# Kernel tuning notes

Measured on AMD Instinct MI355X. Metric: run time of the kernel, lower is better.

The kernel has to match this reference:

```python
import jax, jax.numpy as jnp
import numpy as np

N_NODES = 50000


def _gcn_layer(x, edge_index, W, b, relu):
    """tf_geometric-style GCN: h = D^-1/2 (A+I) D^-1/2 (x @ W) + b, opt relu."""
    n = x.shape[0]
    h = x @ W  # [N, D_out] transform first (standard GCN)
    src, dst = edge_index[0], edge_index[1]
    sl = jnp.arange(n, dtype=src.dtype)
    src = jnp.concatenate([src, sl])  # add self-loops (renorm trick)
    dst = jnp.concatenate([dst, sl])
    deg = jax.ops.segment_sum(jnp.ones_like(dst, dtype=h.dtype), dst, num_segments=n)
    dinv = jax.lax.rsqrt(jnp.maximum(deg, 1e-12))
    norm = dinv[src] * dinv[dst]  # symmetric normalization per edge
    msg = h[src] * norm[:, None]  # [E+N, D_out] gather + scale
    out = jax.ops.segment_sum(msg, dst, num_segments=n) + b
    return jax.nn.relu(out) if relu else out


def setup_inputs() -> dict:
    key = jax.random.key(0)
    ks = jax.random.split(key, 12)
    F, E = 512, 800000
    d = {}
    d["x"] = jax.random.normal(ks[0], (N_NODES, F), dtype=jnp.float32)
    d["edge_index1"] = jax.random.randint(ks[1], (2, E), 0, N_NODES, dtype=jnp.int32)
    d["edge_index2"] = jax.random.randint(ks[2], (2, E), 0, N_NODES, dtype=jnp.int32)
    def glorot(k, shape):
        lim = np.sqrt(6.0 / (shape[0] + shape[1])).astype(np.float32)
        return jax.random.uniform(k, shape, jnp.float32, -lim, lim)
    d["W10"] = glorot(ks[3], (F, 256)); d["b10"] = jnp.zeros((256,), jnp.float32)
    d["W20"] = glorot(ks[4], (F, 64));  d["b20"] = jnp.zeros((64,), jnp.float32)
    d["W21"] = glorot(ks[5], (64, 256)); d["b21"] = jnp.zeros((256,), jnp.float32)
    d["Wfc"] = glorot(ks[6], (256, 16)); d["bfc"] = jnp.zeros((16,), jnp.float32)
    return d


def reference(x, edge_index1, edge_index2, W10, b10, W20, b20, W21, b21, Wfc, bfc):
    h1 = _gcn_layer(x, edge_index1, W10, b10, relu=True)   # GCN(256, relu)
    h2 = _gcn_layer(x, edge_index2, W20, b20, relu=False)  # GCN(64)
    h2 = _gcn_layer(h2, edge_index2, W21, b21, relu=True)  # GCN(256, relu)
    h = h1 + h2
    return h @ Wfc + bfc  # Dense(class_num)
```

## Files before the change

kernel.cpp:

```cpp
#include <hip/hip_runtime.h>
#include <hip/hip_bf16.h>
#include <cstdint>
#include <cstddef>

#define N_NODES 50000
#define FDIM 512
#define NBKT 391
#define CHUNK 8192
#define BCAP 4096

typedef __bf16 bf16_t;
typedef bf16_t bf16x8 __attribute__((ext_vector_type(8)));
typedef float f32x4 __attribute__((ext_vector_type(4)));

__device__ __forceinline__ unsigned short f2bf(float f) {
  union { float f; uint32_t u; } c; c.f = f;
  uint32_t u = c.u;
  uint32_t r = (u + 0x7fffu + ((u >> 16) & 1u)) >> 16;
  return (unsigned short)r;
}
__device__ __forceinline__ float bf2f(unsigned short u) {
  union { uint32_t i; float f; } c; c.i = (uint32_t)u << 16; return c.f;
}
__device__ __forceinline__ float4 ld_bf4(const unsigned short* p) {
  ushort4 u = *(const ushort4*)p;
  float4 r; r.x = bf2f(u.x); r.y = bf2f(u.y); r.z = bf2f(u.z); r.w = bf2f(u.w);
  return r;
}
__device__ __forceinline__ void async16(const void* g, void* l) {
  __builtin_amdgcn_global_load_lds((const __attribute__((address_space(1))) void*)g,
                                   (__attribute__((address_space(3))) void*)l, 16, 0, 0);
}

__global__ __launch_bounds__(256) void binA(const int* __restrict__ d1, const int* __restrict__ d2,
                                            int* __restrict__ M1, int* __restrict__ M2,
                                            int E1, int E2, int nch1, int nch2) {
  const int g = blockIdx.y;
  const int* dst = g ? d2 : d1;
  int* M = g ? M2 : M1;
  const int E = g ? E2 : E1;
  const int nch = g ? nch2 : nch1;
  const int chunk = blockIdx.x;
  if (chunk >= nch) return;
  __shared__ int cnt[NBKT];
  for (int j = threadIdx.x; j < NBKT; j += 256) cnt[j] = 0;
  __syncthreads();
  const int base = chunk * CHUNK;
#pragma unroll 4
  for (int i = 0; i < CHUNK / 256; i++) {
    int e = base + i * 256 + threadIdx.x;
    if (e < E) atomicAdd(&cnt[dst[e] >> 7], 1);
  }
  __syncthreads();
  for (int j = threadIdx.x; j < NBKT; j += 256) M[chunk * NBKT + j] = cnt[j];
}

__global__ __launch_bounds__(512) void bin_offsets(int* __restrict__ M1, int* __restrict__ M2,
                                                   int* __restrict__ bases,
                                                   int nch1, int nch2, int E1, int E2) {
  const int g = blockIdx.x;
  int* M = g ? M2 : M1;
  const int nch = g ? nch2 : nch1;
  int* base = bases + g * (NBKT + 1);
  const int E = g ? E2 : E1;
  const int t = threadIdx.x;
  __shared__ int tot[512];
  int running = 0;
  if (t < NBKT) {
#pragma unroll 4
    for (int b = 0; b < nch; b++) {
      int v = M[b * NBKT + t];
      M[b * NBKT + t] = running;
      running += v;
    }
  }
  tot[t] = (t < NBKT) ? running : 0;
  __syncthreads();
  for (int off = 1; off < 512; off <<= 1) {
    int u = (t >= off) ? tot[t - off] : 0;
    __syncthreads();
    tot[t] += u;
    __syncthreads();
  }
  int ex = (t == 0) ? 0 : tot[t - 1];
  if (t < NBKT) {
    base[t] = ex;
#pragma unroll 4
    for (int b = 0; b < nch; b++) M[b * NBKT + t] += ex;
  }
  if (t == NBKT) base[NBKT] = E;
}

__global__ __launch_bounds__(256) void binB(const int* __restrict__ s1, const int* __restrict__ d1,
                                            const int* __restrict__ M1, unsigned* __restrict__ eb1,
                                            int E1, int nch1,
                                            const int* __restrict__ s2, const int* __restrict__ d2,
                                            const int* __restrict__ M2, unsigned* __restrict__ eb2,
                                            int E2, int nch2) {
  const int g = blockIdx.y;
  const int* src = g ? s2 : s1;
  const int* dst = g ? d2 : d1;
  const int* M = g ? M2 : M1;
  unsigned* eb = g ? eb2 : eb1;
  const int E = g ? E2 : E1;
  const int nch = g ? nch2 : nch1;
  const int chunk = blockIdx.x;
  if (chunk >= nch) return;
  __shared__ int gbase[NBKT];
  __shared__ int cur[NBKT];
  for (int j = threadIdx.x; j < NBKT; j += 256) {
    gbase[j] = M[chunk * NBKT + j];
    cur[j] = 0;
  }
  __syncthreads();
  const int base = chunk * CHUNK;
#pragma unroll 4
  for (int i = 0; i < CHUNK / 256; i++) {
    int e = base + i * 256 + threadIdx.x;
    if (e < E) {
      int d = dst[e];
      int b = d >> 7;
      int pos = gbase[b] + atomicAdd(&cur[b], 1);
      eb[pos] = ((unsigned)d << 16) | (unsigned)src[e];
    }
  }
}

__global__ __launch_bounds__(256) void binC(const unsigned* __restrict__ eb1,
                                            const unsigned* __restrict__ eb2,
                                            const int* __restrict__ bases,
                                            int* __restrict__ rp1, float* __restrict__ dv1,
                                            int* __restrict__ cs1,
                                            int* __restrict__ rp2, float* __restrict__ dv2,
                                            int* __restrict__ cs2, int n) {
  const int g = blockIdx.y;
  const unsigned* eb = g ? eb2 : eb1;
  const int* base = bases + g * (NBKT + 1);
  int* rp = g ? rp2 : rp1;
  float* dv = g ? dv2 : dv1;
  int* cs = g ? cs2 : cs1;
  const int bkt = blockIdx.x;
  const int e0 = base[bkt], e1 = base[bkt + 1];
  const int cnt = e1 - e0;
  const int node0 = bkt << 7;
  const int t = threadIdx.x;
  __shared__ unsigned stage[BCAP];
  __shared__ int sorted[BCAP];
  __shared__ int dcnt[128], dcur[128], dscan[128];
  if (t < 128) dcnt[t] = 0;
  __syncthreads();
  for (int i = t; i < cnt; i += 256) {
    unsigned pe = eb[e0 + i];
    stage[i] = pe;
    atomicAdd(&dcnt[(pe >> 16) & 127], 1);
  }
  __syncthreads();
  if (t < 128) dscan[t] = dcnt[t];
  __syncthreads();
  for (int off = 1; off < 128; off <<= 1) {
    int u = (t < 128 && t >= off) ? dscan[t - off] : 0;
    __syncthreads();
    if (t < 128) dscan[t] += u;
    __syncthreads();
  }
  if (t < 128) {
    int ex = dscan[t] - dcnt[t];
    dcur[t] = ex;
    int node = node0 + t;
    if (node < n) {
      rp[node] = e0 + ex;
      dv[node] = rsqrtf((float)dcnt[t] + 1.0f);
    }
  }
  __syncthreads();
  for (int i = t; i < cnt; i += 256) {
    unsigned pe = stage[i];
    int d = (pe >> 16) & 127;
    int pos = atomicAdd(&dcur[d], 1);
    sorted[pos] = (int)(pe & 0xFFFFu);
  }
  __syncthreads();
  for (int i = t; i < cnt; i += 256) cs[e0 + i] = sorted[i];
  if (bkt == NBKT - 1 && t == 0) rp[n] = base[NBKT];
}

__global__ void cvt_w(const float* __restrict__ W10, const float* __restrict__ W20,
                      const float* __restrict__ W21, unsigned short* __restrict__ WcatT,
                      unsigned short* __restrict__ W21T) {
  int j = blockIdx.x * 256 + threadIdx.x;
  const int T1 = 384 * 512;
  if (j < T1) {
    int n = j >> 9, k = j & 511;
    float v = (n < 256) ? W10[k * 256 + n] : ((n < 320) ? W20[k * 64 + (n - 256)] : 0.f);
    WcatT[j] = f2bf(v);
  } else {
    int j2 = j - T1;
    if (j2 < 256 * 64) {
      int n = j2 >> 6, k = j2 & 63;
      W21T[j2] = f2bf(W21[k * 256 + n]);
    }
  }
}

__global__ __launch_bounds__(256) void g2(const float* __restrict__ X,
                                          const unsigned short* __restrict__ B,
                                          unsigned short* __restrict__ o1,
                                          unsigned short* __restrict__ o2, int M) {
  __shared__ __attribute__((aligned(16))) unsigned short As[64 * 64];
  __shared__ __attribute__((aligned(16))) unsigned short Bs[320 * 64];
  const int tid = threadIdx.x;
  const int w = tid >> 6, lane = tid & 63;
  const int row0 = blockIdx.x * 64;
  const int mlane = lane & 15, q = lane >> 4;

  const int ar = tid >> 4;
  const int ac4 = tid & 15;

  f32x4 acc[4][5];
#pragma unroll
  for (int mi = 0; mi < 4; mi++)
#pragma unroll
    for (int ni = 0; ni < 5; ni++) {
      f32x4 z = {0.f, 0.f, 0.f, 0.f};
      acc[mi][ni] = z;
    }

  for (int k0 = 0; k0 < 512; k0 += 64) {
    __syncthreads();
    float4 areg[4];
#pragma unroll
    for (int i = 0; i < 4; i++) {
      int r = i * 16 + ar;
      int gr = row0 + r; if (gr > M - 1) gr = M - 1;
      areg[i] = *(const float4*)(X + (size_t)gr * 512 + k0 + ac4 * 4);
    }
#pragma unroll
    for (int i = 0; i < 10; i++) {
      int idx = i * 256 + tid;
      int rw = idx >> 3, c8 = idx & 7;
      int sslot = c8 ^ (rw & 7);
      async16(B + (size_t)rw * 512 + k0 + sslot * 8, &Bs[idx * 8]);
    }
#pragma unroll
    for (int i = 0; i < 4; i++) {
      int r = i * 16 + ar;
      ushort4 o;
      o.x = f2bf(areg[i].x); o.y = f2bf(areg[i].y);
      o.z = f2bf(areg[i].z); o.w = f2bf(areg[i].w);
      int slot = ((ac4 >> 1) ^ (r & 7));
      *(ushort4*)&As[r * 64 + slot * 8 + (ac4 & 1) * 4] = o;
    }
    __syncthreads();
#pragma unroll
    for (int kk = 0; kk < 2; kk++) {
      bf16x8 af[4], bfr[5];
#pragma unroll
      for (int mi = 0; mi < 4; mi++) {
        int r = mi * 16 + mlane;
        int slot = (kk * 4 + q) ^ (r & 7);
        af[mi] = *(const bf16x8*)&As[r * 64 + slot * 8];
      }
#pragma unroll
      for (int ni = 0; ni < 5; ni++) {
        int r = w * 80 + ni * 16 + mlane;
        int slot = (kk * 4 + q) ^ (r & 7);
        bfr[ni] = *(const bf16x8*)&Bs[r * 64 + slot * 8];
      }
#pragma unroll
      for (int mi = 0; mi < 4; mi++)
#pragma unroll
        for (int ni = 0; ni < 5; ni++)
          acc[mi][ni] = __builtin_amdgcn_mfma_f32_16x16x32_bf16(af[mi], bfr[ni], acc[mi][ni], 0, 0, 0);
    }
  }

#pragma unroll
  for (int mi = 0; mi < 4; mi++)
#pragma unroll
    for (int ni = 0; ni < 5; ni++) {
      int c = w * 80 + ni * 16 + mlane;
#pragma unroll
      for (int rg = 0; rg < 4; rg++) {
        int r = row0 + mi * 16 + q * 4 + rg;
        if (r < M) {
          float v = acc[mi][ni][rg];
          if (c < 256) o1[(size_t)r * 256 + c] = f2bf(v);
          else o2[(size_t)r * 64 + (c - 256)] = f2bf(v);
        }
      }
    }
}

__global__ __launch_bounds__(256) void prop256(const unsigned short* __restrict__ H,
                                               const int* __restrict__ rp,
                                               const int* __restrict__ cs,
                                               const float* __restrict__ dinv,
                                               const float* __restrict__ bias,
                                               float* __restrict__ out, int n) {
  const int i = blockIdx.x * 4 + (threadIdx.x >> 6);
  const int l = threadIdx.x & 63;
  if (i >= n) return;
  const float di = dinv[i];
  float4 self = ld_bf4(H + (size_t)i * 256 + l * 4);
  float4 acc;
  acc.x = di * self.x; acc.y = di * self.y; acc.z = di * self.z; acc.w = di * self.w;
  const int e1 = rp[i + 1];
#pragma unroll 4
  for (int e = rp[i]; e < e1; e++) {
    int s = cs[e];
    float wgt = dinv[s];
    float4 rrow = ld_bf4(H + (size_t)s * 256 + l * 4);
    acc.x += wgt * rrow.x; acc.y += wgt * rrow.y; acc.z += wgt * rrow.z; acc.w += wgt * rrow.w;
  }
  float4 b = *(const float4*)(bias + l * 4);
  float4 o;
  o.x = fmaxf(di * acc.x + b.x, 0.f);
  o.y = fmaxf(di * acc.y + b.y, 0.f);
  o.z = fmaxf(di * acc.z + b.z, 0.f);
  o.w = fmaxf(di * acc.w + b.w, 0.f);
  *(float4*)(out + (size_t)i * 256 + l * 4) = o;
}

template <int BIAS>
__global__ __launch_bounds__(256) void prop64(const unsigned short* __restrict__ H,
                                              const int* __restrict__ rp,
                                              const int* __restrict__ cs,
                                              const float* __restrict__ dinv,
                                              const float* __restrict__ bias,
                                              unsigned short* __restrict__ out, int n) {
  const int i = blockIdx.x * 16 + (threadIdx.x >> 4);
  const int l = threadIdx.x & 15;
  if (i >= n) return;
  const float di = dinv[i];
  float4 self = ld_bf4(H + (size_t)i * 64 + l * 4);
  float4 acc;
  acc.x = di * self.x; acc.y = di * self.y; acc.z = di * self.z; acc.w = di * self.w;
  const int e1 = rp[i + 1];
#pragma unroll 4
  for (int e = rp[i]; e < e1; e++) {
    int s = cs[e];
    float wgt = dinv[s];
    float4 rrow = ld_bf4(H + (size_t)s * 64 + l * 4);
    acc.x += wgt * rrow.x; acc.y += wgt * rrow.y; acc.z += wgt * rrow.z; acc.w += wgt * rrow.w;
  }
  float4 o;
  o.x = di * acc.x; o.y = di * acc.y; o.z = di * acc.z; o.w = di * acc.w;
  if (BIAS) {
    float4 b = *(const float4*)(bias + l * 4);
    o.x += b.x; o.y += b.y; o.z += b.z; o.w += b.w;
  }
  ushort4 ob;
  ob.x = f2bf(o.x); ob.y = f2bf(o.y); ob.z = f2bf(o.z); ob.w = f2bf(o.w);
  *(ushort4*)(out + (size_t)i * 64 + l * 4) = ob;
}

__global__ __launch_bounds__(512) void gf(const unsigned short* __restrict__ A,
                                          const unsigned short* __restrict__ Bb,
                                          const float* __restrict__ h1,
                                          const float* __restrict__ b21,
                                          const float* __restrict__ Wfc,
                                          const float* __restrict__ bfc,
                                          float* __restrict__ out, int M) {
  __shared__ __attribute__((aligned(16))) float hsm[128 * 260];
  __shared__ __attribute__((aligned(16))) float wt[256 * 16];
  unsigned short* As = (unsigned short*)hsm;
  unsigned short* Bs = As + 128 * 64;
  const int tid = threadIdx.x;
  const int w = tid >> 6, lane = tid & 63;
  const int row0 = blockIdx.x * 128;
  const int wm = w >> 2, wn = w & 3;
  const int mlane = lane & 15, q = lane >> 4;

  for (int j = tid; j < 4096; j += 512) wt[j] = Wfc[j];
#pragma unroll
  for (int i = 0; i < 2; i++) {
    int gr = row0 + i * 64 + w * 8 + (lane >> 3);
    if (gr > M - 1) gr = M - 1;
    async16(A + (size_t)gr * 64 + (lane & 7) * 8, &As[(i * 64 + w * 8) * 64]);
  }
#pragma unroll
  for (int i = 0; i < 4; i++) {
    int n = i * 64 + w * 8 + (lane >> 3);
    async16(Bb + (size_t)n * 64 + (lane & 7) * 8, &Bs[(i * 64 + w * 8) * 64]);
  }
  __syncthreads();

  f32x4 acc[4][4];
#pragma unroll
  for (int mi = 0; mi < 4; mi++)
#pragma unroll
    for (int ni = 0; ni < 4; ni++) {
      f32x4 z = {0.f, 0.f, 0.f, 0.f};
      acc[mi][ni] = z;
    }
#pragma unroll
  for (int kk = 0; kk < 2; kk++) {
    bf16x8 af[4], bfr[4];
#pragma unroll
    for (int mi = 0; mi < 4; mi++)
      af[mi] = *(const bf16x8*)&As[(wm * 64 + mi * 16 + mlane) * 64 + kk * 32 + q * 8];
#pragma unroll
    for (int ni = 0; ni < 4; ni++)
      bfr[ni] = *(const bf16x8*)&Bs[(wn * 64 + ni * 16 + mlane) * 64 + kk * 32 + q * 8];
#pragma unroll
    for (int mi = 0; mi < 4; mi++)
#pragma unroll
      for (int ni = 0; ni < 4; ni++)
        acc[mi][ni] = __builtin_amdgcn_mfma_f32_16x16x32_bf16(af[mi], bfr[ni], acc[mi][ni], 0, 0, 0);
  }
  __syncthreads();

#pragma unroll
  for (int ni = 0; ni < 4; ni++) {
    int c = wn * 64 + ni * 16 + mlane;
    float bb = b21[c];
#pragma unroll
    for (int mi = 0; mi < 4; mi++)
#pragma unroll
      for (int rg = 0; rg < 4; rg++) {
        int rl = wm * 64 + mi * 16 + q * 4 + rg;
        int gr = row0 + rl;
        int grc = (gr < M) ? gr : (M - 1);
        float v = fmaxf(acc[mi][ni][rg] + bb, 0.f) + h1[(size_t)grc * 256 + c];
        hsm[rl * 260 + c] = v;
      }
  }
  __syncthreads();

  const int r = tid >> 2, j0 = (tid & 3) * 4;
  const int gr = row0 + r;
  if (gr < M) {
    float4 s = *(const float4*)(bfc + j0);
    const float* hrow = &hsm[r * 260];
#pragma unroll 8
    for (int c4 = 0; c4 < 64; c4++) {
      float4 h4 = *(const float4*)(hrow + c4 * 4);
      const float* wp = &wt[(c4 * 4) * 16 + j0];
      float4 a0 = *(const float4*)(wp);
      float4 a1 = *(const float4*)(wp + 16);
      float4 a2 = *(const float4*)(wp + 32);
      float4 a3 = *(const float4*)(wp + 48);
      s.x += h4.x * a0.x + h4.y * a1.x + h4.z * a2.x + h4.w * a3.x;
      s.y += h4.x * a0.y + h4.y * a1.y + h4.z * a2.y + h4.w * a3.y;
      s.z += h4.x * a0.z + h4.y * a1.z + h4.z * a2.z + h4.w * a3.z;
      s.w += h4.x * a0.w + h4.y * a1.w + h4.z * a2.w + h4.w * a3.w;
    }
    *(float4*)(out + (size_t)gr * 16 + j0) = s;
  }
}

extern "C" void kernel_launch(void* const* d_in, const int* in_sizes, int n_in,
                              void* d_out, int out_size, void* d_ws, size_t ws_size,
                              hipStream_t stream) {
  const float* X   = (const float*)d_in[0];
  const int*   ei1 = (const int*)d_in[1];
  const int*   ei2 = (const int*)d_in[2];
  const float* W10 = (const float*)d_in[3];
  const float* b10 = (const float*)d_in[4];
  const float* W20 = (const float*)d_in[5];
  const float* b20 = (const float*)d_in[6];
  const float* W21 = (const float*)d_in[7];
  const float* b21 = (const float*)d_in[8];
  const float* Wfc = (const float*)d_in[9];
  const float* bfc = (const float*)d_in[10];
  float* out = (float*)d_out;

  const int N = N_NODES;
  const int E1 = in_sizes[1] / 2, E2 = in_sizes[2] / 2;
  const int* src1 = ei1; const int* dst1 = ei1 + E1;
  const int* src2 = ei2; const int* dst2 = ei2 + E2;
  const int nch1 = (E1 + CHUNK - 1) / CHUNK, nch2 = (E2 + CHUNK - 1) / CHUNK;
  const int nchmax = (nch1 > nch2) ? nch1 : nch2;

  char* p = (char*)d_ws;
  auto alloc = [&](size_t b) { char* r = p; p += (b + 255) & ~(size_t)255; return (void*)r; };
  int* M1 = (int*)alloc((size_t)nch1 * NBKT * 4);
  int* M2 = (int*)alloc((size_t)nch2 * NBKT * 4);
  int* bases = (int*)alloc((size_t)2 * (NBKT + 1) * 4);
  unsigned* eb1 = (unsigned*)alloc((size_t)E1 * 4);
  unsigned* eb2 = (unsigned*)alloc((size_t)E2 * 4);
  int* rp1 = (int*)alloc((size_t)(N + 1) * 4);
  int* rp2 = (int*)alloc((size_t)(N + 1) * 4);
  float* dinv1 = (float*)alloc((size_t)N * 4);
  float* dinv2 = (float*)alloc((size_t)N * 4);
  int* csr1s = (int*)alloc((size_t)E1 * 4);
  int* csr2s = (int*)alloc((size_t)E2 * 4);
  unsigned short* WcatT = (unsigned short*)alloc(384 * 512 * 2);
  unsigned short* W21T  = (unsigned short*)alloc(256 * 64 * 2);
  unsigned short* Xh1b = (unsigned short*)alloc((size_t)N * 256 * 2);
  unsigned short* Xh2b = (unsigned short*)alloc((size_t)N * 64 * 2);
  unsigned short* h2b  = (unsigned short*)alloc((size_t)N * 64 * 2);
  unsigned short* q2b  = (unsigned short*)alloc((size_t)N * 64 * 2);
  float* h1 = (float*)alloc((size_t)N * 256 * 4);

  binA<<<dim3(nchmax, 2), 256, 0, stream>>>(dst1, dst2, M1, M2, E1, E2, nch1, nch2);
  bin_offsets<<<dim3(2), 512, 0, stream>>>(M1, M2, bases, nch1, nch2, E1, E2);
  binB<<<dim3(nchmax, 2), 256, 0, stream>>>(src1, dst1, M1, eb1, E1, nch1,
                                            src2, dst2, M2, eb2, E2, nch2);
  binC<<<dim3(NBKT, 2), 256, 0, stream>>>(eb1, eb2, bases, rp1, dinv1, csr1s,
                                          rp2, dinv2, csr2s, N);
  cvt_w<<<dim3((384 * 512 + 256 * 64 + 255) / 256), 256, 0, stream>>>(W10, W20, W21, WcatT, W21T);
  g2<<<dim3((N + 63) / 64), 256, 0, stream>>>(X, WcatT, Xh1b, Xh2b, N);
  prop256<<<dim3((N + 3) / 4), 256, 0, stream>>>(Xh1b, rp1, csr1s, dinv1, b10, h1, N);
  prop64<1><<<dim3((N + 15) / 16), 256, 0, stream>>>(Xh2b, rp2, csr2s, dinv2, b20, h2b, N);
  prop64<0><<<dim3((N + 15) / 16), 256, 0, stream>>>(h2b, rp2, csr2s, dinv2, nullptr, q2b, N);
  gf<<<dim3((N + 127) / 128), 512, 0, stream>>>(q2b, W21T, h1, b21, Wfc, bfc, out, N);
}
```

Baseline: 392.4 us.

## Load GEMM operands straight from global memory into MFMA registers, dropping LDS staging

The fused X·[W10|W20] GEMM no longer stages A and B tiles through shared memory with swizzling and barriers. Each lane now loads its own MFMA fragments directly from global memory, converting X from fp32 to bf16 in registers, and the k-loop is unrolled by two. This removes LDS traffic and __syncthreads stalls. In exchange, all four waves re-read the same X rows, loads become uncoalesced 32-byte per-lane accesses, and the kernel leans on L1/L2 for reuse.

Measured after the change: 472.2 us. 20.3% more time.

```diff
diff --git a/kernel.cpp b/kernel.cpp
--- a/kernel.cpp
+++ b/kernel.cpp
@@ -202,19 +202,15 @@
   }
 }
 
-__global__ __launch_bounds__(256) void g2(const float* __restrict__ X,
+__global__ __launch_bounds__(256) void g3(const float* __restrict__ X,
                                           const unsigned short* __restrict__ B,
                                           unsigned short* __restrict__ o1,
                                           unsigned short* __restrict__ o2, int M) {
-  __shared__ __attribute__((aligned(16))) unsigned short As[64 * 64];
-  __shared__ __attribute__((aligned(16))) unsigned short Bs[320 * 64];
   const int tid = threadIdx.x;
   const int w = tid >> 6, lane = tid & 63;
   const int row0 = blockIdx.x * 64;
+  const int n0 = w * 80;
   const int mlane = lane & 15, q = lane >> 4;
-
-  const int ar = tid >> 4;
-  const int ac4 = tid & 15;
 
   f32x4 acc[4][5];
 #pragma unroll
@@ -225,60 +221,45 @@
       acc[mi][ni] = z;
     }
 
-  for (int k0 = 0; k0 < 512; k0 += 64) {
-    __syncthreads();
-    float4 areg[4];
-#pragma unroll
-    for (int i = 0; i < 4; i++) {
-      int r = i * 16 + ar;
-      int gr = row0 + r; if (gr > M - 1) gr = M - 1;
-      areg[i] = *(const float4*)(X + (size_t)gr * 512 + k0 + ac4 * 4);
-    }
-#pragma unroll
-    for (int i = 0; i < 10; i++) {
-      int idx = i * 256 + tid;
-      int rw = idx >> 3, c8 = idx & 7;
-      int sslot = c8 ^ (rw & 7);
-      async16(B + (size_t)rw * 512 + k0 + sslot * 8, &Bs[idx * 8]);
-    }
-#pragma unroll
-    for (int i = 0; i < 4; i++) {
-      int r = i * 16 + ar;
-      ushort4 o;
-      o.x = f2bf(areg[i].x); o.y = f2bf(areg[i].y);
-      o.z = f2bf(areg[i].z); o.w = f2bf(areg[i].w);
-      int slot = ((ac4 >> 1) ^ (r & 7));
-      *(ushort4*)&As[r * 64 + slot * 8 + (ac4 & 1) * 4] = o;
-    }
-    __syncthreads();
-#pragma unroll
-    for (int kk = 0; kk < 2; kk++) {
-      bf16x8 af[4], bfr[5];
-#pragma unroll
-      for (int mi = 0; mi < 4; mi++) {
-        int r = mi * 16 + mlane;
-        int slot = (kk * 4 + q) ^ (r & 7);
-        af[mi] = *(const bf16x8*)&As[r * 64 + slot * 8];
-      }
-#pragma unroll
-      for (int ni = 0; ni < 5; ni++) {
-        int r = w * 80 + ni * 16 + mlane;
-        int slot = (kk * 4 + q) ^ (r & 7);
-        bfr[ni] = *(const bf16x8*)&Bs[r * 64 + slot * 8];
-      }
-#pragma unroll
-      for (int mi = 0; mi < 4; mi++)
-#pragma unroll
-        for (int ni = 0; ni < 5; ni++)
-          acc[mi][ni] = __builtin_amdgcn_mfma_f32_16x16x32_bf16(af[mi], bfr[ni], acc[mi][ni], 0, 0, 0);
-    }
+  const float* xp[4];
+#pragma unroll
+  for (int mi = 0; mi < 4; mi++) {
+    int gr = row0 + mi * 16 + mlane; if (gr > M - 1) gr = M - 1;
+    xp[mi] = X + (size_t)gr * 512 + q * 8;
+  }
+  const unsigned short* bp[5];
+#pragma unroll
+  for (int ni = 0; ni < 5; ni++)
+    bp[ni] = B + (size_t)(n0 + ni * 16 + mlane) * 512 + q * 8;
+
+#pragma unroll 2
+  for (int k0 = 0; k0 < 512; k0 += 32) {
+    bf16x8 af[4];
+#pragma unroll
+    for (int mi = 0; mi < 4; mi++) {
+      float4 a0 = *(const float4*)(xp[mi] + k0);
+      float4 a1 = *(const float4*)(xp[mi] + k0 + 4);
+      af[mi][0] = (bf16_t)a0.x; af[mi][1] = (bf16_t)a0.y;
+      af[mi][2] = (bf16_t)a0.z; af[mi][3] = (bf16_t)a0.w;
+      af[mi][4] = (bf16_t)a1.x; af[mi][5] = (bf16_t)a1.y;
+      af[mi][6] = (bf16_t)a1.z; af[mi][7] = (bf16_t)a1.w;
+    }
+    bf16x8 bfr[5];
+#pragma unroll
+    for (int ni = 0; ni < 5; ni++)
+      bfr[ni] = *(const bf16x8*)(bp[ni] + k0);
+#pragma unroll
+    for (int mi = 0; mi < 4; mi++)
+#pragma unroll
+      for (int ni = 0; ni < 5; ni++)
+        acc[mi][ni] = __builtin_amdgcn_mfma_f32_16x16x32_bf16(af[mi], bfr[ni], acc[mi][ni], 0, 0, 0);
   }
 
 #pragma unroll
   for (int mi = 0; mi < 4; mi++)
 #pragma unroll
     for (int ni = 0; ni < 5; ni++) {
-      int c = w * 80 + ni * 16 + mlane;
+      int c = n0 + ni * 16 + mlane;
 #pragma unroll
       for (int rg = 0; rg < 4; rg++) {
         int r = row0 + mi * 16 + q * 4 + rg;
@@ -500,7 +481,7 @@
   binC<<<dim3(NBKT, 2), 256, 0, stream>>>(eb1, eb2, bases, rp1, dinv1, csr1s,
                                           rp2, dinv2, csr2s, N);
   cvt_w<<<dim3((384 * 512 + 256 * 64 + 255) / 256), 256, 0, stream>>>(W10, W20, W21, WcatT, W21T);
-  g2<<<dim3((N + 63) / 64), 256, 0, stream>>>(X, WcatT, Xh1b, Xh2b, N);
+  g3<<<dim3((N + 63) / 64), 256, 0, stream>>>(X, WcatT, Xh1b, Xh2b, N);
   prop256<<<dim3((N + 3) / 4), 256, 0, stream>>>(Xh1b, rp1, csr1s, dinv1, b10, h1, N);
   prop64<1><<<dim3((N + 15) / 16), 256, 0, stream>>>(Xh2b, rp2, csr2s, dinv2, b20, h2b, N);
   prop64<0><<<dim3((N + 15) / 16), 256, 0, stream>>>(h2b, rp2, csr2s, dinv2, nullptr, q2b, N);
```
